# Optimization experiments

Hardware: AMD Instinct MI355X
Metric: run time of the kernel (lower is better)

The kernel has to match this reference:

```python
import jax, jax.numpy as jnp
import numpy as np

N = 131072   # nodes (flattened batch)
SI, VI = 128, 64   # in_dims
SO, VO = 128, 64   # out_dims
HD = 128           # h_dim


def setup_inputs() -> dict:
    key = jax.random.key(0)
    ks = jax.random.split(key, 8)
    scale = lambda fan_in: 1.0 / np.sqrt(fan_in)
    return {
        "s": jax.random.normal(ks[0], (N, SI), dtype=jnp.float32),
        "V": jax.random.normal(ks[1], (N, VI, 3), dtype=jnp.float32),
        # Linear(vi, h_dim, bias=False): weight [h_dim, vi]
        "W_h": jax.random.uniform(ks[2], (HD, VI), jnp.float32, -scale(VI), scale(VI)),
        # Linear(h_dim, vo, bias=False): weight [vo, h_dim]
        "W_V": jax.random.uniform(ks[3], (VO, HD), jnp.float32, -scale(HD), scale(HD)),
        # Linear(si + h_dim, so)
        "W_s_w": jax.random.uniform(ks[4], (SO, SI + HD), jnp.float32, -scale(SI + HD), scale(SI + HD)),
        "W_s_b": jax.random.uniform(ks[5], (SO,), jnp.float32, -scale(SI + HD), scale(SI + HD)),
        # Linear(so, vo) gate
        "W_g_w": jax.random.uniform(ks[6], (VO, SO), jnp.float32, -scale(SO), scale(SO)),
        "W_g_b": jax.random.uniform(ks[7], (VO,), jnp.float32, -scale(SO), scale(SO)),
    }


def reference(s, V, W_h, W_V, W_s_w, W_s_b, W_g_w, W_g_b):
    # Vh: contract vector-channel dim vi, keep 3 spatial dims -> [N, h_dim, 3]
    Vh = jnp.einsum("nvc,hv->nhc", V, W_h)
    # L2 norm over the 3 spatial dims -> [N, h_dim]
    Vh_norm = jnp.sqrt(jnp.sum(Vh * Vh, axis=-1))
    # V_out: [N, vo, 3]
    V_out = jnp.einsum("nhc,oh->noc", Vh, W_V)
    # scalar path: concat + linear + relu -> [N, so]
    s_cat = jnp.concatenate([s, Vh_norm], axis=-1)
    s_out = jax.nn.relu(s_cat @ W_s_w.T + W_s_b)
    # vector gate: sigmoid(Linear(s_out)) broadcast over spatial dim
    gate = jax.nn.sigmoid(s_out @ W_g_w.T + W_g_b)[..., None]  # [N, vo, 1]
    V_out = V_out * gate
    return s_out, V_out
```

## Files before the change

kernel.cpp:

```cpp
#include <hip/hip_runtime.h>
#include <hip/hip_bf16.h>
#include <math.h>

#define NNODES 131072
#define BN 32

typedef __attribute__((ext_vector_type(8))) short bf16x8;
typedef __attribute__((ext_vector_type(4))) float f32x4;

__device__ short g_w[49152];
__device__ short g_wc[4096];

__device__ __forceinline__ short f2b(float f) {
  union { float f; unsigned u; } x; x.f = f;
  unsigned r = x.u + 0x7fffu + ((x.u >> 16) & 1u);
  return (short)(r >> 16);
}
__device__ __forceinline__ short c2b(float f) {
  __hip_bfloat16 h = __float2bfloat16(f);
  return *reinterpret_cast<short*>(&h);
}

__global__ void prep_kernel(const float* __restrict__ W_h, const float* __restrict__ W_V,
                            const float* __restrict__ W_s_w, const float* __restrict__ W_g_w) {
  int b = blockIdx.x;
  if (b < 48) {
    int i4 = (b * 256 + threadIdx.x) * 4;
    const float* src;
    if (i4 < 8192)       src = W_h   + i4;
    else if (i4 < 40960) src = W_s_w + (i4 - 8192);
    else                 src = W_g_w + (i4 - 40960);
    float4 q = *(const float4*)src;
    short4 p;
    p.x = f2b(q.x); p.y = f2b(q.y); p.z = f2b(q.z); p.w = f2b(q.w);
    *(short4*)(g_w + i4) = p;
  } else {
    int gid = (b - 48) * 256 + threadIdx.x;
    int o  = gid >> 4;
    int v0 = (gid & 15) * 4;
    float a0 = 0.f, a1 = 0.f, a2 = 0.f, a3 = 0.f;
    #pragma unroll 8
    for (int h = 0; h < 128; ++h) {
      float wv = W_V[o * 128 + h];
      float4 wh = *(const float4*)(W_h + h * 64 + v0);
      a0 += wv * wh.x; a1 += wv * wh.y; a2 += wv * wh.z; a3 += wv * wh.w;
    }
    short4 p;
    p.x = f2b(a0); p.y = f2b(a1); p.z = f2b(a2); p.w = f2b(a3);
    *(short4*)(g_wc + o * 64 + v0) = p;
  }
}


__global__ __launch_bounds__(256, 4)
void gvp_kernel(const float* __restrict__ s_in, const float* __restrict__ V_in,
                const float* __restrict__ W_s_b, const float* __restrict__ W_g_b,
                float* __restrict__ s_out_g, float* __restrict__ V_out_g)
{
  __shared__ __align__(16) char smem[36864];
  char*  const Vt   = smem;
  float* const VST  = (float*)smem;
  char*  const SC   = smem + 12288;
  char*  const NORM = smem + 20480;
  char*  const SOUT = smem + 28672;

  const short* const g_wh = g_w;
  const short* const g_ws = g_w + 8192;
  const short* const g_wg = g_w + 40960;

  const int t    = threadIdx.x;
  const int lane = t & 63;
  const int w    = t >> 6;
  const int l15  = lane & 15;
  const int lk8  = (lane >> 4) << 3;
  const int r4   = (lane >> 4) << 2;
  const long n0  = (long)blockIdx.x * BN;

  {
    const int nl = t >> 3;
    const int vg = t & 7;
    const int v0 = vg << 3;
    const float* vp = V_in + (n0 + nl) * 192 + v0 * 3;
    float4 q0 = *(const float4*)(vp);
    float4 q1 = *(const float4*)(vp + 4);
    float4 q2 = *(const float4*)(vp + 8);
    float4 q3 = *(const float4*)(vp + 12);
    float4 q4 = *(const float4*)(vp + 16);
    float4 q5 = *(const float4*)(vp + 20);
    float fl[24];
    *(float4*)(fl)      = q0; *(float4*)(fl + 4)  = q1;
    *(float4*)(fl + 8)  = q2; *(float4*)(fl + 12) = q3;
    *(float4*)(fl + 16) = q4; *(float4*)(fl + 20) = q5;
    #pragma unroll
    for (int c = 0; c < 3; ++c) {
      int row = (c << 5) + nl;
      bf16x8 p;
      #pragma unroll
      for (int j = 0; j < 8; ++j) p[j] = c2b(fl[j * 3 + c]);
      unsigned a = (unsigned)(row * 128) + (((unsigned)(v0 * 2)) ^ (unsigned)((row & 7) << 4));
      *(bf16x8*)(Vt + a) = p;
    }
  }
  {
    const int nl = t >> 3;
    const int kg = t & 7;
    const int k0 = kg << 4;
    const float* sp = s_in + (n0 + nl) * 128 + k0;
    float4 q0 = *(const float4*)(sp);
    float4 q1 = *(const float4*)(sp + 4);
    float4 q2 = *(const float4*)(sp + 8);
    float4 q3 = *(const float4*)(sp + 12);
    bf16x8 pa, pb;
    pa[0] = c2b(q0.x); pa[1] = c2b(q0.y); pa[2] = c2b(q0.z); pa[3] = c2b(q0.w);
    pa[4] = c2b(q1.x); pa[5] = c2b(q1.y); pa[6] = c2b(q1.z); pa[7] = c2b(q1.w);
    pb[0] = c2b(q2.x); pb[1] = c2b(q2.y); pb[2] = c2b(q2.z); pb[3] = c2b(q2.w);
    pb[4] = c2b(q3.x); pb[5] = c2b(q3.y); pb[6] = c2b(q3.z); pb[7] = c2b(q3.w);
    unsigned sw = (unsigned)((nl & 7) << 4);
    unsigned aA = (unsigned)(nl * 256) + (((unsigned)(k0 * 2)) ^ sw);
    unsigned aB = (unsigned)(nl * 256) + (((unsigned)(k0 * 2 + 16)) ^ sw);
    *(bf16x8*)(SC + aA) = pa;
    *(bf16x8*)(SC + aB) = pb;
  }
  __syncthreads();

  f32x4 acc1[6][2];
  f32x4 acc2[6];
  #pragma unroll
  for (int rt = 0; rt < 6; ++rt) {
    f32x4 z = {0.f, 0.f, 0.f, 0.f};
    acc1[rt][0] = z; acc1[rt][1] = z; acc2[rt] = z;
  }
  {
    bf16x8 bf1[2][2];
    #pragma unroll
    for (int cc = 0; cc < 2; ++cc) {
      int h = ((2 * w + cc) << 4) + l15;
      #pragma unroll
      for (int ks = 0; ks < 2; ++ks)
        bf1[cc][ks] = *(const bf16x8*)(g_wh + h * 64 + (ks << 5) + lk8);
    }
    bf16x8 bc[2];
    {
      int o = (w << 4) + l15;
      bc[0] = *(const bf16x8*)(g_wc + o * 64 + lk8);
      bc[1] = *(const bf16x8*)(g_wc + o * 64 + 32 + lk8);
    }
    #pragma unroll
    for (int rt = 0; rt < 6; ++rt) {
      int row = (rt << 4) + l15;
      unsigned sw = (unsigned)((row & 7) << 4);
      bf16x8 af0 = *(const bf16x8*)(Vt + row * 128 + (((unsigned)(lk8 * 2)) ^ sw));
      bf16x8 af1 = *(const bf16x8*)(Vt + row * 128 + (((unsigned)((32 + lk8) * 2)) ^ sw));
      #pragma unroll
      for (int cc = 0; cc < 2; ++cc) {
        acc1[rt][cc] = __builtin_amdgcn_mfma_f32_16x16x32_bf16(af0, bf1[cc][0], acc1[rt][cc], 0, 0, 0);
        acc1[rt][cc] = __builtin_amdgcn_mfma_f32_16x16x32_bf16(af1, bf1[cc][1], acc1[rt][cc], 0, 0, 0);
      }
      acc2[rt] = __builtin_amdgcn_mfma_f32_16x16x32_bf16(af0, bc[0], acc2[rt], 0, 0, 0);
      acc2[rt] = __builtin_amdgcn_mfma_f32_16x16x32_bf16(af1, bc[1], acc2[rt], 0, 0, 0);
    }
  }

  #pragma unroll
  for (int cc = 0; cc < 2; ++cc) {
    int col = ((2 * w + cc) << 4) + l15;
    #pragma unroll
    for (int rt = 0; rt < 2; ++rt) {
      #pragma unroll
      for (int i = 0; i < 4; ++i) {
        int nl = (rt << 4) + r4 + i;
        float x0 = acc1[rt][cc][i];
        float x1 = acc1[rt + 2][cc][i];
        float x2 = acc1[rt + 4][cc][i];
        float nrm = sqrtf(x0 * x0 + x1 * x1 + x2 * x2);
        unsigned a = (unsigned)(nl * 256) + (((unsigned)(col * 2)) ^ (unsigned)((nl & 7) << 4));
        *(short*)(NORM + a) = c2b(nrm);
      }
    }
  }
  __syncthreads();

  f32x4 acc3[2][2];
  {
    f32x4 z = {0.f, 0.f, 0.f, 0.f};
    acc3[0][0] = z; acc3[0][1] = z; acc3[1][0] = z; acc3[1][1] = z;
  }
  #pragma unroll
  for (int ks = 0; ks < 8; ++ks) {
    bf16x8 b3[2];
    #pragma unroll
    for (int cc = 0; cc < 2; ++cc) {
      int o = (w << 5) + (cc << 4) + l15;
      b3[cc] = *(const bf16x8*)(g_ws + o * 256 + (ks << 5) + lk8);
    }
    #pragma unroll
    for (int rt = 0; rt < 2; ++rt) {
      int row = (rt << 4) + l15;
      unsigned sw = (unsigned)((row & 7) << 4);
      bf16x8 a;
      if (ks < 4) {
        a = *(const bf16x8*)(SC + row * 256 + (((unsigned)(((ks << 5) + lk8) * 2)) ^ sw));
      } else {
        a = *(const bf16x8*)(NORM + row * 256 + (((unsigned)((((ks - 4) << 5) + lk8) * 2)) ^ sw));
      }
      acc3[rt][0] = __builtin_amdgcn_mfma_f32_16x16x32_bf16(a, b3[0], acc3[rt][0], 0, 0, 0);
      acc3[rt][1] = __builtin_amdgcn_mfma_f32_16x16x32_bf16(a, b3[1], acc3[rt][1], 0, 0, 0);
    }
  }

  {
    float bias0 = W_s_b[(w << 5) + l15];
    float bias1 = W_s_b[(w << 5) + 16 + l15];
    #pragma unroll
    for (int rt = 0; rt < 2; ++rt) {
      #pragma unroll
      for (int i = 0; i < 4; ++i) {
        int row = (rt << 4) + r4 + i;
        unsigned sw = (unsigned)((row & 7) << 4);
        float v0 = fmaxf(acc3[rt][0][i] + bias0, 0.0f);
        float v1 = fmaxf(acc3[rt][1][i] + bias1, 0.0f);
        int col0 = (w << 5) + l15;
        s_out_g[(n0 + row) * 128 + col0]      = v0;
        s_out_g[(n0 + row) * 128 + col0 + 16] = v1;
        unsigned a0 = (unsigned)(row * 256) + (((unsigned)(col0 * 2)) ^ sw);
        unsigned a1 = (unsigned)(row * 256) + (((unsigned)((col0 + 16) * 2)) ^ sw);
        *(short*)(SOUT + a0) = c2b(v0);
        *(short*)(SOUT + a1) = c2b(v1);
      }
    }
  }
  __syncthreads();

  f32x4 acc4[2];
  { f32x4 z = {0.f, 0.f, 0.f, 0.f}; acc4[0] = z; acc4[1] = z; }
  {
    int o = (w << 4) + l15;
    #pragma unroll
    for (int ks = 0; ks < 4; ++ks) {
      bf16x8 b4 = *(const bf16x8*)(g_wg + o * 128 + (ks << 5) + lk8);
      #pragma unroll
      for (int rt = 0; rt < 2; ++rt) {
        int row = (rt << 4) + l15;
        bf16x8 a = *(const bf16x8*)(SOUT + row * 256 +
                     (((unsigned)(((ks << 5) + lk8) * 2)) ^ ((unsigned)((row & 7) << 4))));
        acc4[rt] = __builtin_amdgcn_mfma_f32_16x16x32_bf16(a, b4, acc4[rt], 0, 0, 0);
      }
    }
  }

  {
    int col = (w << 4) + l15;
    float biasg = W_g_b[col];
    #pragma unroll
    for (int nlg = 0; nlg < 2; ++nlg) {
      #pragma unroll
      for (int i = 0; i < 4; ++i) {
        int nl = (nlg << 4) + r4 + i;
        float x = acc4[nlg][i] + biasg;
        float sg = 1.0f / (1.0f + __expf(-x));
        VST[nl * 192 + col * 3 + 0] = acc2[nlg][i]     * sg;
        VST[nl * 192 + col * 3 + 1] = acc2[2 + nlg][i] * sg;
        VST[nl * 192 + col * 3 + 2] = acc2[4 + nlg][i] * sg;
      }
    }
  }
  __syncthreads();

  {
    float4* Vo = (float4*)(V_out_g + n0 * 192);
    const float4* Vs = (const float4*)VST;
    #pragma unroll
    for (int i = 0; i < 6; ++i) {
      int idx = t + 256 * i;
      Vo[idx] = Vs[idx];
    }
  }
}

extern "C" void kernel_launch(void* const* d_in, const int* in_sizes, int n_in,
                              void* d_out, int out_size, void* d_ws, size_t ws_size,
                              hipStream_t stream) {
  const float* s_in  = (const float*)d_in[0];
  const float* V_in  = (const float*)d_in[1];
  const float* W_h   = (const float*)d_in[2];
  const float* W_V   = (const float*)d_in[3];
  const float* W_s_w = (const float*)d_in[4];
  const float* W_s_b = (const float*)d_in[5];
  const float* W_g_w = (const float*)d_in[6];
  const float* W_g_b = (const float*)d_in[7];
  float* out = (float*)d_out;
  float* s_out_g = out;
  float* V_out_g = out + (size_t)NNODES * 128;
  hipLaunchKernelGGL(prep_kernel, dim3(52), dim3(256), 0, stream,
                     W_h, W_V, W_s_w, W_g_w);
  hipLaunchKernelGGL(gvp_kernel, dim3(NNODES / BN), dim3(256), 0, stream,
                     s_in, V_in, W_s_b, W_g_b, s_out_g, V_out_g);
}
```

Baseline: 110.2 us.

## Shrink LDS footprint and defer vector-output GEMM to raise occupancy

Shared memory shrinks from 36 KB to 28 KB by merging the scalar and norm buffers into one concatenated tile, aliasing the s_out buffer onto it, and staging V output in two 16-node halves with a swizzled layout. The W_V·W_h MFMA accumulation moves after the scalar GEMM so fewer accumulators are live at once, and launch bounds rise from 4 to 5 blocks per CU. The aim is higher occupancy to hide global memory latency. The cost is extra __syncthreads barriers, a second pass over the V tile in LDS, and possible register spills under the tighter launch bound.

```diff
diff --git a/kernel.cpp b/kernel.cpp
--- a/kernel.cpp
+++ b/kernel.cpp
@@ -52,17 +52,16 @@
 }
 
 
-__global__ __launch_bounds__(256, 4)
+__global__ __launch_bounds__(256, 5)
 void gvp_kernel(const float* __restrict__ s_in, const float* __restrict__ V_in,
                 const float* __restrict__ W_s_b, const float* __restrict__ W_g_b,
                 float* __restrict__ s_out_g, float* __restrict__ V_out_g)
 {
-  __shared__ __align__(16) char smem[36864];
-  char*  const Vt   = smem;
-  float* const VST  = (float*)smem;
-  char*  const SC   = smem + 12288;
-  char*  const NORM = smem + 20480;
-  char*  const SOUT = smem + 28672;
+  __shared__ __align__(16) char smem[28672];
+  char* const Vt   = smem;
+  char* const VSTb = smem;
+  char* const SCN  = smem + 12288;
+  char* const SOUT = smem + 12288;
 
   const short* const g_wh = g_w;
   const short* const g_ws = g_w + 8192;
@@ -81,16 +80,9 @@
     const int vg = t & 7;
     const int v0 = vg << 3;
     const float* vp = V_in + (n0 + nl) * 192 + v0 * 3;
-    float4 q0 = *(const float4*)(vp);
-    float4 q1 = *(const float4*)(vp + 4);
-    float4 q2 = *(const float4*)(vp + 8);
-    float4 q3 = *(const float4*)(vp + 12);
-    float4 q4 = *(const float4*)(vp + 16);
-    float4 q5 = *(const float4*)(vp + 20);
     float fl[24];
-    *(float4*)(fl)      = q0; *(float4*)(fl + 4)  = q1;
-    *(float4*)(fl + 8)  = q2; *(float4*)(fl + 12) = q3;
-    *(float4*)(fl + 16) = q4; *(float4*)(fl + 20) = q5;
+    #pragma unroll
+    for (int i = 0; i < 6; ++i) *(float4*)(fl + 4 * i) = *(const float4*)(vp + 4 * i);
     #pragma unroll
     for (int c = 0; c < 3; ++c) {
       int row = (c << 5) + nl;
@@ -116,19 +108,16 @@
     pb[0] = c2b(q2.x); pb[1] = c2b(q2.y); pb[2] = c2b(q2.z); pb[3] = c2b(q2.w);
     pb[4] = c2b(q3.x); pb[5] = c2b(q3.y); pb[6] = c2b(q3.z); pb[7] = c2b(q3.w);
     unsigned sw = (unsigned)((nl & 7) << 4);
-    unsigned aA = (unsigned)(nl * 256) + (((unsigned)(k0 * 2)) ^ sw);
-    unsigned aB = (unsigned)(nl * 256) + (((unsigned)(k0 * 2 + 16)) ^ sw);
-    *(bf16x8*)(SC + aA) = pa;
-    *(bf16x8*)(SC + aB) = pb;
+    *(bf16x8*)(SCN + nl * 512 + (((unsigned)(k0 * 2)) ^ sw))      = pa;
+    *(bf16x8*)(SCN + nl * 512 + (((unsigned)(k0 * 2 + 16)) ^ sw)) = pb;
   }
   __syncthreads();
 
   f32x4 acc1[6][2];
-  f32x4 acc2[6];
   #pragma unroll
   for (int rt = 0; rt < 6; ++rt) {
     f32x4 z = {0.f, 0.f, 0.f, 0.f};
-    acc1[rt][0] = z; acc1[rt][1] = z; acc2[rt] = z;
+    acc1[rt][0] = z; acc1[rt][1] = z;
   }
   {
     bf16x8 bf1[2][2];
@@ -138,12 +127,6 @@
       #pragma unroll
       for (int ks = 0; ks < 2; ++ks)
         bf1[cc][ks] = *(const bf16x8*)(g_wh + h * 64 + (ks << 5) + lk8);
-    }
-    bf16x8 bc[2];
-    {
-      int o = (w << 4) + l15;
-      bc[0] = *(const bf16x8*)(g_wc + o * 64 + lk8);
-      bc[1] = *(const bf16x8*)(g_wc + o * 64 + 32 + lk8);
     }
     #pragma unroll
     for (int rt = 0; rt < 6; ++rt) {
@@ -156,8 +139,6 @@
         acc1[rt][cc] = __builtin_amdgcn_mfma_f32_16x16x32_bf16(af0, bf1[cc][0], acc1[rt][cc], 0, 0, 0);
         acc1[rt][cc] = __builtin_amdgcn_mfma_f32_16x16x32_bf16(af1, bf1[cc][1], acc1[rt][cc], 0, 0, 0);
       }
-      acc2[rt] = __builtin_amdgcn_mfma_f32_16x16x32_bf16(af0, bc[0], acc2[rt], 0, 0, 0);
-      acc2[rt] = __builtin_amdgcn_mfma_f32_16x16x32_bf16(af1, bc[1], acc2[rt], 0, 0, 0);
     }
   }
 
@@ -173,8 +154,9 @@
         float x1 = acc1[rt + 2][cc][i];
         float x2 = acc1[rt + 4][cc][i];
         float nrm = sqrtf(x0 * x0 + x1 * x1 + x2 * x2);
-        unsigned a = (unsigned)(nl * 256) + (((unsigned)(col * 2)) ^ (unsigned)((nl & 7) << 4));
-        *(short*)(NORM + a) = c2b(nrm);
+        int k = 128 + col;
+        unsigned a = (unsigned)(nl * 512) + (((unsigned)(k * 2)) ^ (unsigned)((nl & 7) << 4));
+        *(short*)(SCN + a) = c2b(nrm);
       }
     }
   }
@@ -197,17 +179,33 @@
     for (int rt = 0; rt < 2; ++rt) {
       int row = (rt << 4) + l15;
       unsigned sw = (unsigned)((row & 7) << 4);
-      bf16x8 a;
-      if (ks < 4) {
-        a = *(const bf16x8*)(SC + row * 256 + (((unsigned)(((ks << 5) + lk8) * 2)) ^ sw));
-      } else {
-        a = *(const bf16x8*)(NORM + row * 256 + (((unsigned)((((ks - 4) << 5) + lk8) * 2)) ^ sw));
-      }
+      bf16x8 a = *(const bf16x8*)(SCN + row * 512 +
+                   (((unsigned)(((ks << 5) + lk8) * 2)) ^ sw));
       acc3[rt][0] = __builtin_amdgcn_mfma_f32_16x16x32_bf16(a, b3[0], acc3[rt][0], 0, 0, 0);
       acc3[rt][1] = __builtin_amdgcn_mfma_f32_16x16x32_bf16(a, b3[1], acc3[rt][1], 0, 0, 0);
     }
   }
 
+  f32x4 acc2[6];
+  #pragma unroll
+  for (int rt = 0; rt < 6; ++rt) { f32x4 z = {0.f,0.f,0.f,0.f}; acc2[rt] = z; }
+  {
+    bf16x8 bc[2];
+    int o = (w << 4) + l15;
+    bc[0] = *(const bf16x8*)(g_wc + o * 64 + lk8);
+    bc[1] = *(const bf16x8*)(g_wc + o * 64 + 32 + lk8);
+    #pragma unroll
+    for (int rt = 0; rt < 6; ++rt) {
+      int row = (rt << 4) + l15;
+      unsigned sw = (unsigned)((row & 7) << 4);
+      bf16x8 af0 = *(const bf16x8*)(Vt + row * 128 + (((unsigned)(lk8 * 2)) ^ sw));
+      bf16x8 af1 = *(const bf16x8*)(Vt + row * 128 + (((unsigned)((32 + lk8) * 2)) ^ sw));
+      acc2[rt] = __builtin_amdgcn_mfma_f32_16x16x32_bf16(af0, bc[0], acc2[rt], 0, 0, 0);
+      acc2[rt] = __builtin_amdgcn_mfma_f32_16x16x32_bf16(af1, bc[1], acc2[rt], 0, 0, 0);
+    }
+  }
+
+  float so[2][2][4];
   {
     float bias0 = W_s_b[(w << 5) + l15];
     float bias1 = W_s_b[(w << 5) + 16 + l15];
@@ -216,17 +214,28 @@
       #pragma unroll
       for (int i = 0; i < 4; ++i) {
         int row = (rt << 4) + r4 + i;
-        unsigned sw = (unsigned)((row & 7) << 4);
         float v0 = fmaxf(acc3[rt][0][i] + bias0, 0.0f);
         float v1 = fmaxf(acc3[rt][1][i] + bias1, 0.0f);
+        so[rt][0][i] = v0; so[rt][1][i] = v1;
         int col0 = (w << 5) + l15;
         s_out_g[(n0 + row) * 128 + col0]      = v0;
         s_out_g[(n0 + row) * 128 + col0 + 16] = v1;
-        unsigned a0 = (unsigned)(row * 256) + (((unsigned)(col0 * 2)) ^ sw);
-        unsigned a1 = (unsigned)(row * 256) + (((unsigned)((col0 + 16) * 2)) ^ sw);
-        *(short*)(SOUT + a0) = c2b(v0);
-        *(short*)(SOUT + a1) = c2b(v1);
-      }
+      }
+    }
+  }
+  __syncthreads();
+
+  #pragma unroll
+  for (int rt = 0; rt < 2; ++rt) {
+    #pragma unroll
+    for (int i = 0; i < 4; ++i) {
+      int row = (rt << 4) + r4 + i;
+      unsigned sw = (unsigned)((row & 7) << 4);
+      int col0 = (w << 5) + l15;
+      unsigned a0 = (unsigned)(row * 256) + (((unsigned)(col0 * 2)) ^ sw);
+      unsigned a1 = (unsigned)(row * 256) + (((unsigned)((col0 + 16) * 2)) ^ sw);
+      *(short*)(SOUT + a0) = c2b(so[rt][0][i]);
+      *(short*)(SOUT + a1) = c2b(so[rt][1][i]);
     }
   }
   __syncthreads();
@@ -247,33 +256,46 @@
       }
     }
   }
-
-  {
-    int col = (w << 4) + l15;
-    float biasg = W_g_b[col];
-    #pragma unroll
-    for (int nlg = 0; nlg < 2; ++nlg) {
-      #pragma unroll
-      for (int i = 0; i < 4; ++i) {
-        int nl = (nlg << 4) + r4 + i;
-        float x = acc4[nlg][i] + biasg;
-        float sg = 1.0f / (1.0f + __expf(-x));
-        VST[nl * 192 + col * 3 + 0] = acc2[nlg][i]     * sg;
-        VST[nl * 192 + col * 3 + 1] = acc2[2 + nlg][i] * sg;
-        VST[nl * 192 + col * 3 + 2] = acc2[4 + nlg][i] * sg;
-      }
-    }
-  }
-  __syncthreads();
-
-  {
-    float4* Vo = (float4*)(V_out_g + n0 * 192);
-    const float4* Vs = (const float4*)VST;
-    #pragma unroll
-    for (int i = 0; i < 6; ++i) {
-      int idx = t + 256 * i;
-      Vo[idx] = Vs[idx];
-    }
+  float sg[2][4];
+  {
+    float biasg = W_g_b[(w << 4) + l15];
+    #pragma unroll
+    for (int nlg = 0; nlg < 2; ++nlg)
+      #pragma unroll
+      for (int i = 0; i < 4; ++i)
+        sg[nlg][i] = 1.0f / (1.0f + __expf(-(acc4[nlg][i] + biasg)));
+  }
+
+  #pragma unroll
+  for (int r = 0; r < 2; ++r) {
+    {
+      int col = (w << 4) + l15;
+      #pragma unroll
+      for (int c = 0; c < 3; ++c) {
+        #pragma unroll
+        for (int i = 0; i < 4; ++i) {
+          int nl_rel = r4 + i;
+          unsigned sw = (unsigned)(nl_rel << 4);
+          unsigned base = (unsigned)(nl_rel * 768);
+          *(float*)(VSTb + base + (((unsigned)((col * 3 + c) * 4)) ^ sw)) =
+              acc2[c * 2 + r][i] * sg[r][i];
+        }
+      }
+    }
+    __syncthreads();
+    {
+      float4* Vo = (float4*)(V_out_g + (n0 + (long)(r << 4)) * 192);
+      #pragma unroll
+      for (int j = 0; j < 3; ++j) {
+        int f = j * 256 + t;
+        int nl_rel = (f * 1366) >> 16;
+        int rem = f - nl_rel * 48;
+        float4 q = *(const float4*)(VSTb + nl_rel * 768 +
+                     (((unsigned)(rem * 16)) ^ ((unsigned)(nl_rel << 4))));
+        Vo[f] = q;
+      }
+    }
+    if (r == 0) __syncthreads();
   }
 }
 
```

Measured after the change: 110.8 us. About the same (+0.6%).
